# Kernel tuning notes

Hardware: AMD Instinct MI355X
Metric: run time of the kernel (lower is better)

Reference implementation:

```python
import jax, jax.numpy as jnp
import numpy as np

NUM_EMBEDDINGS = 4096
EMBEDDING_DIM = 64
COMMITMENT_COST = 0.25
DECAY = 0.99
EPS = 1e-5


def setup_inputs() -> dict:
    key = jax.random.key(0)
    k1, k2, k3 = jax.random.split(key, 3)
    z = jax.random.normal(k1, (32, 1024, EMBEDDING_DIM), dtype=jnp.float32)
    # codebook initialized uniform(-1/K, 1/K) in the original; use small-scale normal-equivalent uniform
    embedding = jax.random.uniform(k2, (NUM_EMBEDDINGS, EMBEDDING_DIM), dtype=jnp.float32,
                                   minval=-1.0 / NUM_EMBEDDINGS, maxval=1.0 / NUM_EMBEDDINGS)
    ema_cluster_size = jnp.zeros((NUM_EMBEDDINGS,), dtype=jnp.float32)
    ema_w = embedding  # buffer initialized as a clone of the weight
    return {"z": z, "embedding": embedding, "ema_cluster_size": ema_cluster_size, "ema_w": ema_w}


def reference(z, embedding, ema_cluster_size, ema_w):
    B, T, D = z.shape
    K = embedding.shape[0]
    z_flat = z.reshape(-1, D)  # [N, D], N = B*T

    # squared L2 distances: ||z||^2 + ||e||^2 - 2 z e^T  -> [N, K]
    d = (jnp.sum(z_flat * z_flat, axis=1, keepdims=True)
         + jnp.sum(embedding * embedding, axis=1)
         - 2.0 * jnp.einsum('nd,kd->nk', z_flat, embedding))
    indices = jnp.argmin(d, axis=1)  # [N]

    z_q = embedding[indices].reshape(B, T, D)

    # EMA codebook update (training path); segment_sum == one-hot matmul, without
    # materializing the [N, K] one-hot matrix.
    counts = jax.ops.segment_sum(jnp.ones_like(indices, dtype=jnp.float32), indices,
                                 num_segments=K)  # encodings.sum(0)
    dw = jax.ops.segment_sum(z_flat, indices, num_segments=K)  # (z_flat^T @ encodings)^T -> [K, D]
    new_cluster_size = DECAY * ema_cluster_size + (1.0 - DECAY) * counts
    new_ema_w = DECAY * ema_w + (1.0 - DECAY) * dw
    n = jnp.sum(new_cluster_size)
    cluster_size = (new_cluster_size + EPS) / (n + K * EPS) * n
    new_embedding = new_ema_w / cluster_size[:, None]

    commitment_loss = COMMITMENT_COST * jnp.mean((z - jax.lax.stop_gradient(z_q)) ** 2)
    z_q_st = z + jax.lax.stop_gradient(z_q - z)  # straight-through estimator
    return (z_q_st, indices.reshape(B, T), commitment_loss,
            new_embedding, new_cluster_size, new_ema_w)
```

## Files before the change

### kernel.cpp

```cpp
#include <hip/hip_runtime.h>

#define N_ROWS 32768
#define K_EMB  4096
#define D_DIM  64
#define MARGIN 5e-4f
#define CAND_CAP 16
#define NCHUNKY 16

#define WS_EE     0
#define WS_BEST   4096
#define WS_IDX    69632
#define WS_COUNTS 102400
#define WS_DW     106496
#define WS_LOSS   368640
#define WS_N      368641
#define F_BHI     368644
#define F_BLO     499716
#define F_ROWMIN  630788
#define F_CNT     663556
#define F_CAND    696324
#define WS_NEED_BYTES ((size_t)(696324 + 32768 * CAND_CAP) * 4)

#define O_ZQ    0
#define O_IDX   2097152
#define O_LOSS  2129920
#define O_EMB   2129921
#define O_CS    2392065
#define O_EMAW  2396161

typedef __attribute__((ext_vector_type(8))) short short8;
typedef __attribute__((ext_vector_type(4))) float f32x4;

__device__ __forceinline__ unsigned short f2bf(float f) {
    unsigned u = __float_as_uint(f);
    unsigned r = (u + 0x7FFFu + ((u >> 16) & 1u)) >> 16;
    return (unsigned short)r;
}
__device__ __forceinline__ unsigned keyf(float f) {
    unsigned u = __float_as_uint(f);
    return (u & 0x80000000u) ? ~u : (u | 0x80000000u);
}
__device__ __forceinline__ float keyinv(unsigned k) {
    unsigned u = (k & 0x80000000u) ? (k ^ 0x80000000u) : ~k;
    return __uint_as_float(u);
}

__global__ void k_ee(const float* __restrict__ emb, float* __restrict__ ee) {
    int k = blockIdx.x * 256 + threadIdx.x;
    const float4* e4 = (const float4*)(emb + (size_t)k * D_DIM);
    float s0 = 0.f, s1 = 0.f, s2 = 0.f, s3 = 0.f;
#pragma unroll
    for (int i = 0; i < 16; ++i) {
        float4 v = e4[i];
        s0 = fmaf(v.x, v.x, s0);
        s1 = fmaf(v.y, v.y, s1);
        s2 = fmaf(v.z, v.z, s2);
        s3 = fmaf(v.w, v.w, s3);
    }
    ee[k] = (s0 + s1) + (s2 + s3);
}

__global__ void k_prep(const float* __restrict__ emb, float* __restrict__ ee,
                       unsigned short* __restrict__ bhi)
{
    int k = blockIdx.x * 256 + threadIdx.x;
    const float4* e4 = (const float4*)(emb + (size_t)k * D_DIM);
    float s0 = 0.f, s1 = 0.f, s2 = 0.f, s3 = 0.f;
    unsigned short* bh = bhi + (size_t)k * D_DIM;
#pragma unroll
    for (int i = 0; i < 16; ++i) {
        float4 v = e4[i];
        s0 = fmaf(v.x, v.x, s0);
        s1 = fmaf(v.y, v.y, s1);
        s2 = fmaf(v.z, v.z, s2);
        s3 = fmaf(v.w, v.w, s3);
        bh[4 * i + 0] = f2bf(v.x);
        bh[4 * i + 1] = f2bf(v.y);
        bh[4 * i + 2] = f2bf(v.z);
        bh[4 * i + 3] = f2bf(v.w);
    }
    ee[k] = (s0 + s1) + (s2 + s3);
}

template <int PASS>
__global__ __launch_bounds__(256, 3) void k_mfma_pass(
    const float* __restrict__ z, const unsigned short* __restrict__ bhi,
    const float* __restrict__ ee,
    unsigned* __restrict__ rowmin, unsigned* __restrict__ cnt, int* __restrict__ cand)
{
    const int tid  = threadIdx.x;
    const int lane = tid & 63, wave = tid >> 6;
    const int lrow = lane & 15, lgrp = lane >> 4;
    const int row0  = blockIdx.x * 256 + wave * 64;
    const int kbase = blockIdx.y * (K_EMB / NCHUNKY);

    short8 Ah[4][2];
#pragma unroll
    for (int s = 0; s < 4; ++s) {
#pragma unroll
        for (int t = 0; t < 2; ++t) {
            const float* zp = z + (size_t)(row0 + s * 16 + lrow) * D_DIM + t * 32 + lgrp * 8;
            float4 f0 = *(const float4*)zp;
            float4 f1 = *(const float4*)(zp + 4);
            float zf[8] = {f0.x, f0.y, f0.z, f0.w, f1.x, f1.y, f1.z, f1.w};
            short8 h;
#pragma unroll
            for (int j = 0; j < 8; ++j) h[j] = (short)f2bf(zf[j]);
            Ah[s][t] = h;
        }
    }

    float track[4][4];
#pragma unroll
    for (int s = 0; s < 4; ++s)
#pragma unroll
        for (int r = 0; r < 4; ++r) {
            track[s][r] = (PASS == 1)
                ? 3.4e38f
                : keyinv(rowmin[row0 + s * 16 + lgrp * 4 + r]) + MARGIN;
        }

#pragma unroll 2
    for (int kt = 0; kt < (K_EMB / NCHUNKY) / 32; ++kt) {
        const int k0 = kbase + kt * 32;
        short8 B0[2], B1[2];
        float  ev[2];
#pragma unroll
        for (int u = 0; u < 2; ++u) {
            const unsigned short* bp = bhi + (size_t)(k0 + u * 16 + lrow) * D_DIM + lgrp * 8;
            B0[u] = *(const short8*)bp;
            B1[u] = *(const short8*)(bp + 32);
            ev[u] = ee[k0 + u * 16 + lrow];
        }
#pragma unroll
        for (int s = 0; s < 4; ++s) {
#pragma unroll
            for (int u = 0; u < 2; ++u) {
                f32x4 acc = {0.f, 0.f, 0.f, 0.f};
                acc = __builtin_amdgcn_mfma_f32_16x16x32_bf16(Ah[s][0], B0[u], acc, 0, 0, 0);
                acc = __builtin_amdgcn_mfma_f32_16x16x32_bf16(Ah[s][1], B1[u], acc, 0, 0, 0);
#pragma unroll
                for (int r = 0; r < 4; ++r) {
                    float sv = fmaf(-2.0f, acc[r], ev[u]);
                    if (PASS == 1) {
                        track[s][r] = fminf(track[s][r], sv);
                    } else {
                        if (sv < track[s][r]) {
                            int row = row0 + s * 16 + lgrp * 4 + r;
                            unsigned slot = atomicAdd(&cnt[row], 1u);
                            if (slot < (unsigned)CAND_CAP)
                                cand[(size_t)row * CAND_CAP + slot] = k0 + u * 16 + lrow;
                        }
                    }
                }
            }
        }
    }

    if (PASS == 1) {
#pragma unroll
        for (int s = 0; s < 4; ++s)
#pragma unroll
            for (int r = 0; r < 4; ++r) {
                float v = track[s][r];
                v = fminf(v, __shfl_xor(v, 1));
                v = fminf(v, __shfl_xor(v, 2));
                v = fminf(v, __shfl_xor(v, 4));
                v = fminf(v, __shfl_xor(v, 8));
                if (lrow == 0)
                    atomicMin(&rowmin[row0 + s * 16 + lgrp * 4 + r], keyf(v));
            }
    }
}

__global__ void k_refine(const float* __restrict__ z, const float* __restrict__ emb,
                         const float* __restrict__ ee, const unsigned* __restrict__ cnt,
                         const int* __restrict__ cand, unsigned long long* __restrict__ best)
{
    int row = blockIdx.x * 256 + threadIdx.x;
    const float4* zp = (const float4*)(z + (size_t)row * D_DIM);

    float s0 = 0.f, s1 = 0.f, s2 = 0.f, s3 = 0.f;
#pragma unroll
    for (int i = 0; i < 16; ++i) {
        float4 v = zp[i];
        s0 = fmaf(v.x, v.x, s0);
        s1 = fmaf(v.y, v.y, s1);
        s2 = fmaf(v.z, v.z, s2);
        s3 = fmaf(v.w, v.w, s3);
    }
    const float zz = (s0 + s1) + (s2 + s3);

    int c = (int)cnt[row];
    if (c > CAND_CAP) c = CAND_CAP;
    unsigned long long bk = 0xFFFFFFFFFFFFFFFFull;
    for (int i = 0; i < c; ++i) {
        int k = cand[(size_t)row * CAND_CAP + i];
        const float4* ep = (const float4*)(emb + (size_t)k * D_DIM);
        float d0 = 0.f, d1 = 0.f, d2 = 0.f, d3 = 0.f;
#pragma unroll
        for (int j = 0; j < 16; ++j) {
            float4 zv = zp[j];
            float4 ev = ep[j];
            d0 = fmaf(zv.x, ev.x, d0);
            d1 = fmaf(zv.y, ev.y, d1);
            d2 = fmaf(zv.z, ev.z, d2);
            d3 = fmaf(zv.w, ev.w, d3);
        }
        float dot = (d0 + d1) + (d2 + d3);
        float dv  = fmaf(-2.0f, dot, zz + ee[k]);
        unsigned long long key =
            ((unsigned long long)__float_as_uint(dv) << 32) | (unsigned)k;
        bk = (key < bk) ? key : bk;
    }
    best[row] = bk;
}

#define NCHUNK_FB 16
#define KC_FB     (K_EMB / NCHUNK_FB)
__global__ __launch_bounds__(256) void k_argmin_fb(
    const float* __restrict__ z, const float* __restrict__ emb,
    const float* __restrict__ ee, unsigned long long* __restrict__ best)
{
    const int n  = blockIdx.x * 256 + threadIdx.x;
    const int c  = blockIdx.y;
    const int k0 = c * KC_FB;

    float4 zr[16];
    const float4* zp = (const float4*)(z + (size_t)n * D_DIM);
#pragma unroll
    for (int i = 0; i < 16; ++i) zr[i] = zp[i];

    float s0 = 0.f, s1 = 0.f, s2 = 0.f, s3 = 0.f;
#pragma unroll
    for (int i = 0; i < 16; ++i) {
        s0 = fmaf(zr[i].x, zr[i].x, s0);
        s1 = fmaf(zr[i].y, zr[i].y, s1);
        s2 = fmaf(zr[i].z, zr[i].z, s2);
        s3 = fmaf(zr[i].w, zr[i].w, s3);
    }
    const float zz = (s0 + s1) + (s2 + s3);

    const float4* ep  = (const float4*)(emb + (size_t)k0 * D_DIM);
    const float*  eep = ee + k0;

    float bestv = 3.4e38f;
    int   bi    = 0;
#pragma unroll 2
    for (int kk = 0; kk < KC_FB; ++kk) {
        float d0 = 0.f, d1 = 0.f, d2 = 0.f, d3 = 0.f;
#pragma unroll
        for (int i = 0; i < 16; ++i) {
            float4 ev = ep[kk * 16 + i];
            d0 = fmaf(zr[i].x, ev.x, d0);
            d1 = fmaf(zr[i].y, ev.y, d1);
            d2 = fmaf(zr[i].z, ev.z, d2);
            d3 = fmaf(zr[i].w, ev.w, d3);
        }
        float dot = (d0 + d1) + (d2 + d3);
        float dv = fmaf(-2.0f, dot, zz + eep[kk]);
        if (dv < bestv) { bestv = dv; bi = kk; }
    }
    unsigned long long key =
        ((unsigned long long)__float_as_uint(bestv) << 32) | (unsigned)(k0 + bi);
    atomicMin(best + n, key);
}

__global__ void k_finish(const unsigned long long* __restrict__ best,
                         int* __restrict__ idxbuf, float* __restrict__ oidx)
{
    int n = blockIdx.x * 256 + threadIdx.x;
    int bi = (int)(best[n] & 0xFFFFFFFFull);
    idxbuf[n] = bi;
    oidx[n]   = (float)bi;
}

__global__ void k_scatter(const float* __restrict__ z, const float* __restrict__ emb,
                          const int* __restrict__ idxbuf, float* __restrict__ out_zq,
                          float* __restrict__ counts, float* __restrict__ dw,
                          float* __restrict__ lossacc)
{
    int t = blockIdx.x * 256 + threadIdx.x;
    float acc = 0.f;
#pragma unroll
    for (int i = 0; i < 16; ++i) {
        int e = t + i * 131072;
        int nrow = e >> 6, d = e & 63;
        int k = idxbuf[nrow];
        float zv  = z[e];
        float evv = emb[(size_t)k * D_DIM + d];
        out_zq[e] = zv + (evv - zv);
        float diff = zv - evv;
        acc = fmaf(diff, diff, acc);
        atomicAdd(&dw[(size_t)k * D_DIM + d], zv);
        if (d == 0) atomicAdd(&counts[k], 1.0f);
    }
    __shared__ float red[256];
    red[threadIdx.x] = acc;
    __syncthreads();
    for (int s = 128; s > 0; s >>= 1) {
        if (threadIdx.x < s) red[threadIdx.x] += red[threadIdx.x + s];
        __syncthreads();
    }
    if (threadIdx.x == 0) atomicAdd(lossacc, red[0]);
}

__global__ void k_stats(const float* __restrict__ ema_cs, const float* __restrict__ counts,
                        const float* __restrict__ lossacc, float* __restrict__ out_cs,
                        float* __restrict__ out_loss, float* __restrict__ ws_n)
{
    __shared__ float red[256];
    float local = 0.f;
    for (int k = threadIdx.x; k < K_EMB; k += 256) {
        float v = 0.99f * ema_cs[k] + 0.01f * counts[k];
        out_cs[k] = v;
        local += v;
    }
    red[threadIdx.x] = local;
    __syncthreads();
    for (int s = 128; s > 0; s >>= 1) {
        if (threadIdx.x < s) red[threadIdx.x] += red[threadIdx.x + s];
        __syncthreads();
    }
    if (threadIdx.x == 0) {
        ws_n[0] = red[0];
        out_loss[0] = 0.25f * (lossacc[0] / 2097152.0f);
    }
}

__global__ void k_emb(const float* __restrict__ ema_w, const float* __restrict__ dw,
                      const float* __restrict__ out_cs, const float* __restrict__ ws_n,
                      float* __restrict__ out_emb, float* __restrict__ out_emaw)
{
    int e = blockIdx.x * 256 + threadIdx.x;
    int k = e >> 6;
    float nv = ws_n[0];
    float w  = 0.99f * ema_w[e] + 0.01f * dw[e];
    out_emaw[e] = w;
    float cs = (out_cs[k] + 1e-5f) / (nv + 0.04096f) * nv;
    out_emb[e] = w / cs;
}

extern "C" void kernel_launch(void* const* d_in, const int* in_sizes, int n_in,
                              void* d_out, int out_size, void* d_ws, size_t ws_size,
                              hipStream_t stream)
{
    const float* z      = (const float*)d_in[0];
    const float* emb    = (const float*)d_in[1];
    const float* ema_cs = (const float*)d_in[2];
    const float* ema_w  = (const float*)d_in[3];

    float* out   = (float*)d_out;
    float* o_zq  = out + O_ZQ;
    float* o_idx = out + O_IDX;
    float* o_ls  = out + O_LOSS;
    float* o_em  = out + O_EMB;
    float* o_cs  = out + O_CS;
    float* o_ew  = out + O_EMAW;

    float* w      = (float*)d_ws;
    float* ee     = w + WS_EE;
    unsigned long long* best = (unsigned long long*)(w + WS_BEST);
    int*   idxbuf = (int*)(w + WS_IDX);
    float* counts = w + WS_COUNTS;
    float* dw     = w + WS_DW;
    float* lossa  = w + WS_LOSS;
    float* ws_n   = w + WS_N;

    hipMemsetAsync((char*)d_ws + (size_t)WS_BEST * 4, 0xFF, (size_t)N_ROWS * 8, stream);
    hipMemsetAsync((char*)d_ws + (size_t)WS_COUNTS * 4, 0,
                   (size_t)(WS_N + 1 - WS_COUNTS) * 4, stream);

    if (ws_size >= WS_NEED_BYTES) {
        unsigned short* bhi = (unsigned short*)(w + F_BHI);
        unsigned* rowmin    = (unsigned*)(w + F_ROWMIN);
        unsigned* cnt       = (unsigned*)(w + F_CNT);
        int*      cand      = (int*)(w + F_CAND);

        hipMemsetAsync((char*)d_ws + (size_t)F_ROWMIN * 4, 0xFF, (size_t)N_ROWS * 4, stream);
        hipMemsetAsync((char*)d_ws + (size_t)F_CNT * 4, 0, (size_t)N_ROWS * 4, stream);

        k_prep<<<K_EMB / 256, 256, 0, stream>>>(emb, ee, bhi);
        k_mfma_pass<1><<<dim3(N_ROWS / 256, NCHUNKY), 256, 0, stream>>>(z, bhi, ee,
                                                                        rowmin, cnt, cand);
        k_mfma_pass<2><<<dim3(N_ROWS / 256, NCHUNKY), 256, 0, stream>>>(z, bhi, ee,
                                                                        rowmin, cnt, cand);
        k_refine<<<N_ROWS / 256, 256, 0, stream>>>(z, emb, ee, cnt, cand, best);
    } else {
        k_ee<<<K_EMB / 256, 256, 0, stream>>>(emb, ee);
        k_argmin_fb<<<dim3(N_ROWS / 256, NCHUNK_FB), 256, 0, stream>>>(z, emb, ee, best);
    }

    k_finish<<<N_ROWS / 256, 256, 0, stream>>>(best, idxbuf, o_idx);
    k_scatter<<<512, 256, 0, stream>>>(z, emb, idxbuf, o_zq, counts, dw, lossa);
    k_stats<<<1, 256, 0, stream>>>(ema_cs, counts, lossa, o_cs, o_ls, ws_n);
    k_emb<<<(K_EMB * D_DIM) / 256, 256, 0, stream>>>(ema_w, dw, o_cs, ws_n, o_em, o_ew);
}
```

Measured before the change: 185.2 us.

## Stage codebook chunk in swizzled LDS and fold norm into MFMA accumulator init

Each block now loads its 256-row bf16 codebook chunk and the scaled norms into shared memory once, using an XOR swizzle to avoid bank conflicts. The inner loop then reads B fragments from LDS instead of global memory. The MFMA accumulator is seeded with -0.5*||e||^2, so the per-element fma is dropped and tracking switches from a min to a max of the negated half-distance. This adds a __syncthreads, 32KB of LDS per block that may cut occupancy under launch_bounds(256,3), and the sign and scale inversion must stay consistent between the two passes.

```diff
diff --git a/kernel.cpp b/kernel.cpp
--- a/kernel.cpp
+++ b/kernel.cpp
@@ -6,6 +6,7 @@
 #define MARGIN 5e-4f
 #define CAND_CAP 16
 #define NCHUNKY 16
+#define KC_CH   (K_EMB / NCHUNKY)
 
 #define WS_EE     0
 #define WS_BEST   4096
@@ -88,11 +89,28 @@
     const float* __restrict__ ee,
     unsigned* __restrict__ rowmin, unsigned* __restrict__ cnt, int* __restrict__ cand)
 {
+    __shared__ unsigned short lds_b[KC_CH * 64];
+    __shared__ float lds_e2[KC_CH];
+
     const int tid  = threadIdx.x;
     const int lane = tid & 63, wave = tid >> 6;
     const int lrow = lane & 15, lgrp = lane >> 4;
     const int row0  = blockIdx.x * 256 + wave * 64;
-    const int kbase = blockIdx.y * (K_EMB / NCHUNKY);
+    const int kbase = blockIdx.y * KC_CH;
+
+    {
+        const short8* gsrc = (const short8*)(bhi + (size_t)kbase * D_DIM);
+        short8 v[8];
+#pragma unroll
+        for (int j = 0; j < 8; ++j) v[j] = gsrc[tid + j * 256];
+        const int s_slot = tid & 7, c0 = tid >> 3;
+#pragma unroll
+        for (int j = 0; j < 8; ++j) {
+            int c = c0 + j * 32;
+            *(short8*)&lds_b[c * 64 + ((s_slot ^ (c & 7)) << 3)] = v[j];
+        }
+        if (tid < KC_CH) lds_e2[tid] = -0.5f * ee[kbase + tid];
+    }
 
     short8 Ah[4][2];
 #pragma unroll
@@ -116,40 +134,42 @@
 #pragma unroll
         for (int r = 0; r < 4; ++r) {
             track[s][r] = (PASS == 1)
-                ? 3.4e38f
-                : keyinv(rowmin[row0 + s * 16 + lgrp * 4 + r]) + MARGIN;
-        }
-
+                ? -3.4e38f
+                : -0.5f * (keyinv(rowmin[row0 + s * 16 + lgrp * 4 + r]) + MARGIN);
+        }
+
+    __syncthreads();
+
+    const int swz = lrow & 7;
 #pragma unroll 2
-    for (int kt = 0; kt < (K_EMB / NCHUNKY) / 32; ++kt) {
-        const int k0 = kbase + kt * 32;
+    for (int kt = 0; kt < KC_CH / 32; ++kt) {
         short8 B0[2], B1[2];
-        float  ev[2];
+        float  e2[2];
 #pragma unroll
         for (int u = 0; u < 2; ++u) {
-            const unsigned short* bp = bhi + (size_t)(k0 + u * 16 + lrow) * D_DIM + lgrp * 8;
-            B0[u] = *(const short8*)bp;
-            B1[u] = *(const short8*)(bp + 32);
-            ev[u] = ee[k0 + u * 16 + lrow];
+            const int c = kt * 32 + u * 16 + lrow;
+            B0[u] = *(const short8*)&lds_b[c * 64 + ((lgrp ^ swz) << 3)];
+            B1[u] = *(const short8*)&lds_b[c * 64 + (((lgrp + 4) ^ swz) << 3)];
+            e2[u] = lds_e2[c];
         }
 #pragma unroll
         for (int s = 0; s < 4; ++s) {
 #pragma unroll
             for (int u = 0; u < 2; ++u) {
-                f32x4 acc = {0.f, 0.f, 0.f, 0.f};
+                f32x4 acc = {e2[u], e2[u], e2[u], e2[u]};
                 acc = __builtin_amdgcn_mfma_f32_16x16x32_bf16(Ah[s][0], B0[u], acc, 0, 0, 0);
                 acc = __builtin_amdgcn_mfma_f32_16x16x32_bf16(Ah[s][1], B1[u], acc, 0, 0, 0);
 #pragma unroll
                 for (int r = 0; r < 4; ++r) {
-                    float sv = fmaf(-2.0f, acc[r], ev[u]);
                     if (PASS == 1) {
-                        track[s][r] = fminf(track[s][r], sv);
+                        track[s][r] = fmaxf(track[s][r], acc[r]);
                     } else {
-                        if (sv < track[s][r]) {
+                        if (acc[r] > track[s][r]) {
                             int row = row0 + s * 16 + lgrp * 4 + r;
                             unsigned slot = atomicAdd(&cnt[row], 1u);
                             if (slot < (unsigned)CAND_CAP)
-                                cand[(size_t)row * CAND_CAP + slot] = k0 + u * 16 + lrow;
+                                cand[(size_t)row * CAND_CAP + slot] =
+                                    kbase + kt * 32 + u * 16 + lrow;
                         }
                     }
                 }
@@ -163,12 +183,12 @@
 #pragma unroll
             for (int r = 0; r < 4; ++r) {
                 float v = track[s][r];
-                v = fminf(v, __shfl_xor(v, 1));
-                v = fminf(v, __shfl_xor(v, 2));
-                v = fminf(v, __shfl_xor(v, 4));
-                v = fminf(v, __shfl_xor(v, 8));
+                v = fmaxf(v, __shfl_xor(v, 1));
+                v = fmaxf(v, __shfl_xor(v, 2));
+                v = fmaxf(v, __shfl_xor(v, 4));
+                v = fmaxf(v, __shfl_xor(v, 8));
                 if (lrow == 0)
-                    atomicMin(&rowmin[row0 + s * 16 + lgrp * 4 + r], keyf(v));
+                    atomicMin(&rowmin[row0 + s * 16 + lgrp * 4 + r], keyf(-2.0f * v));
             }
     }
 }
```

After: 160.5 us. -13.3%, faster.
